# Optimization experiments

Measured on AMD Instinct MI355X. Metric: run time of the kernel, lower is better.

The kernel has to match this reference:

```python
import jax, jax.numpy as jnp
import numpy as np

B, S, E = 2, 2048, 1024
H, KV = 16, 4
D = E // H            # head_dim = 64
N_REP = H // KV       # 4
WIN = 256             # window_size
KV_DIM = KV * D       # 256


def setup_inputs() -> dict:
    key = jax.random.key(0)
    ks = jax.random.split(key, 10)
    sc_e = 1.0 / np.sqrt(E)
    return {
        "x":  jax.random.normal(ks[0], (B, S, E), jnp.float32),
        # weights stored as [in, out] (transposed torch Linear weight)
        "wq": jax.random.normal(ks[1], (E, E), jnp.float32) * sc_e,
        "bq": jax.random.normal(ks[2], (E,), jnp.float32) * 0.01,
        "wk": jax.random.normal(ks[3], (E, KV_DIM), jnp.float32) * sc_e,
        "bk": jax.random.normal(ks[4], (KV_DIM,), jnp.float32) * 0.01,
        "wv": jax.random.normal(ks[5], (E, KV_DIM), jnp.float32) * sc_e,
        "bv": jax.random.normal(ks[6], (KV_DIM,), jnp.float32) * 0.01,
        "wo": jax.random.normal(ks[7], (E, E), jnp.float32) * sc_e,
        "bo": jax.random.normal(ks[8], (E,), jnp.float32) * 0.01,
    }


def reference(x, wq, bq, wk, bk, wv, bv, wo, bo):
    b, s, _ = x.shape
    q = (x @ wq + bq).reshape(b, s, H, D).transpose(0, 2, 1, 3)    # [B,H,S,D]
    k = (x @ wk + bk).reshape(b, s, KV, D).transpose(0, 2, 1, 3)   # [B,KV,S,D]
    v = (x @ wv + bv).reshape(b, s, KV, D).transpose(0, 2, 1, 3)
    # repeat_kv: each kv head repeated N_REP times consecutively
    k = jnp.repeat(k, N_REP, axis=1)                               # [B,H,S,D]
    v = jnp.repeat(v, N_REP, axis=1)
    scores = jnp.einsum("bhqd,bhkd->bhqk", q, k) * (D ** -0.5)    # [B,H,S,S]
    i = jnp.arange(s)[:, None]
    j = jnp.arange(s)[None, :]
    masked = (j > i) | ((i - j) > WIN)  # True = masked (causal sliding window)
    scores = jnp.where(masked[None, None], -jnp.inf, scores)
    attn = jax.nn.softmax(scores, axis=-1)
    ctx = jnp.einsum("bhqk,bhkd->bhqd", attn, v)                   # [B,H,S,D]
    ctx = ctx.transpose(0, 2, 1, 3).reshape(b, s, E)
    return ctx @ wo + bo
```

## Files before the change

### kernel.cpp

```cpp
#include <hip/hip_runtime.h>
#include <stdint.h>

typedef unsigned short u16;
typedef __attribute__((ext_vector_type(8))) __bf16 bf16x8;
typedef __attribute__((ext_vector_type(4))) __bf16 bf16x4;
typedef __attribute__((ext_vector_type(4))) float f32x4;

#define S_LEN 2048
#define EMB   1024
#define NH    16
#define NKV   4
#define HD    64
#define WIN   256
#define NB    2
#define MROWS (NB * S_LEN)
#define PPAD  72

__device__ __forceinline__ u16 f2bf(float f) {
    uint32_t u = __float_as_uint(f);
    uint32_t r = (u + 0x7FFFu + ((u >> 16) & 1u)) >> 16;
    return (u16)r;
}

__device__ __forceinline__ float fast_exp2(float x) {
#if __has_builtin(__builtin_amdgcn_exp2f)
    return __builtin_amdgcn_exp2f(x);
#else
    float r; asm("v_exp_f32 %0, %1" : "=v"(r) : "v"(x)); return r;
#endif
}

__device__ __forceinline__ void gload16(const void* g, void* l) {
    __builtin_amdgcn_global_load_lds(
        (const __attribute__((address_space(1))) uint32_t*)(uintptr_t)g,
        (__attribute__((address_space(3))) uint32_t*)(uintptr_t)l,
        16, 0, 0);
}

__device__ __forceinline__ void transpose_job64(const float* __restrict__ in,
                                                u16* __restrict__ out,
                                                int R, int C, int bx, int by, int tid) {
    __shared__ float t[64][33];
    int c0 = bx * 32, r0 = by * 64;
    int tx = tid & 31, ty = tid >> 5;
#pragma unroll
    for (int j = 0; j < 64; j += 8)
        t[ty + j][tx] = in[(size_t)(r0 + ty + j) * C + (c0 + tx)];
    __syncthreads();
#pragma unroll
    for (int j = 0; j < 32; j += 8) {
        int c = j + ty;
        uint32_t v = f2bf(t[2 * tx][c]) | ((uint32_t)f2bf(t[2 * tx + 1][c]) << 16);
        *(uint32_t*)(out + (size_t)(c0 + c) * R + r0 + 2 * tx) = v;
    }
}

__global__ __launch_bounds__(256) void prep_kernel(
    const float* __restrict__ x,  const float* __restrict__ wq,
    const float* __restrict__ wk, const float* __restrict__ wv,
    const float* __restrict__ wo,
    u16* __restrict__ xb, u16* __restrict__ wqt, u16* __restrict__ wkt,
    u16* __restrict__ wvt, u16* __restrict__ wot) {
    int bid = blockIdx.x, tid = threadIdx.x;
    if (bid < 2048) {
        int i = bid * 256 + tid;
        const float4* p = (const float4*)x + (size_t)i * 2;
        float4 a = p[0], b = p[1];
        uint4 q;
        q.x = f2bf(a.x) | ((uint32_t)f2bf(a.y) << 16);
        q.y = f2bf(a.z) | ((uint32_t)f2bf(a.w) << 16);
        q.z = f2bf(b.x) | ((uint32_t)f2bf(b.y) << 16);
        q.w = f2bf(b.z) | ((uint32_t)f2bf(b.w) << 16);
        ((uint4*)xb)[i] = q;
    } else if (bid < 2560) {
        int lb = bid - 2048;  transpose_job64(wq, wqt, EMB, EMB, lb & 31, lb >> 5, tid);
    } else if (bid < 2688) {
        int lb = bid - 2560;  transpose_job64(wk, wkt, EMB, 256, lb & 7, lb >> 3, tid);
    } else if (bid < 2816) {
        int lb = bid - 2688;  transpose_job64(wv, wvt, EMB, 256, lb & 7, lb >> 3, tid);
    } else {
        int lb = bid - 2816;  transpose_job64(wo, wot, EMB, EMB, lb & 31, lb >> 5, tid);
    }
}

__device__ __forceinline__ void gemm_core64(const __bf16* __restrict__ A, const __bf16* __restrict__ Bt,
                                            int K, int m0, int n0r,
                                            __bf16 (*As)[64 * 64], __bf16 (*Bs)[128 * 64],
                                            f32x4 (&acc)[2][4], int tid) {
    const int lane = tid & 63, w = tid >> 6;
    const int wr = w >> 1, wc = w & 1;
    const int r = lane & 15, g = lane >> 4;

    auto stage = [&](int buf, int k0) {
#pragma unroll
        for (int i = 0; i < 2; ++i) {
            int chunk = (w * 2 + i) * 64 + lane;
            int row = chunk >> 3, cc = chunk & 7;
            gload16(A + (size_t)(m0 + row) * K + k0 + cc * 8, &As[buf][(w * 2 + i) * 512]);
        }
#pragma unroll
        for (int i = 0; i < 4; ++i) {
            int chunk = (w * 4 + i) * 64 + lane;
            int row = chunk >> 3, cc = chunk & 7;
            gload16(Bt + (size_t)(n0r + row) * K + k0 + cc * 8, &Bs[buf][(w * 4 + i) * 512]);
        }
    };

    stage(0, 0);
    __syncthreads();
    for (int k0 = 0; k0 < K; k0 += 64) {
        int cur = (k0 >> 6) & 1;
        if (k0 + 64 < K) stage(cur ^ 1, k0 + 64);
        bf16x8 af[2][2], bfr[4][2];
#pragma unroll
        for (int mf = 0; mf < 2; ++mf)
#pragma unroll
            for (int kk = 0; kk < 2; ++kk)
                af[mf][kk] = *(const bf16x8*)(&As[cur][(wr * 32 + mf * 16 + r) * 64 + kk * 32 + g * 8]);
#pragma unroll
        for (int nf = 0; nf < 4; ++nf)
#pragma unroll
            for (int kk = 0; kk < 2; ++kk)
                bfr[nf][kk] = *(const bf16x8*)(&Bs[cur][(wc * 64 + nf * 16 + r) * 64 + kk * 32 + g * 8]);
#pragma unroll
        for (int mf = 0; mf < 2; ++mf)
#pragma unroll
            for (int nf = 0; nf < 4; ++nf)
#pragma unroll
                for (int kk = 0; kk < 2; ++kk)
                    acc[mf][nf] = __builtin_amdgcn_mfma_f32_16x16x32_bf16(
                        af[mf][kk], bfr[nf][kk], acc[mf][nf], 0, 0, 0);
        __syncthreads();
    }
}

__global__ __launch_bounds__(256, 3) void gemm_qkv_kernel(
    const __bf16* __restrict__ xb, const __bf16* __restrict__ wqt,
    const __bf16* __restrict__ wkt, const __bf16* __restrict__ wvt,
    const float* __restrict__ bq, const float* __restrict__ bk, const float* __restrict__ bv,
    __bf16* __restrict__ Qb, __bf16* __restrict__ Kb, __bf16* __restrict__ Vblk) {
    __shared__ __align__(16) __bf16 As[2][64 * 64];
    __shared__ __align__(16) __bf16 Bs[2][128 * 64];
    int tid = threadIdx.x;
    int wg = (blockIdx.x & 7) * 96 + (blockIdx.x >> 3);
    int n0 = (wg % 12) * 128, m0 = (wg / 12) * 64;

    const __bf16* Bt; int n0r; const float* bias; int mode;
    if (n0 < 1024)      { Bt = wqt; n0r = n0;        bias = bq; mode = 0; }
    else if (n0 < 1280) { Bt = wkt; n0r = n0 - 1024; bias = bk; mode = 1; }
    else                { Bt = wvt; n0r = n0 - 1280; bias = bv; mode = 2; }

    f32x4 acc[2][4];
    f32x4 z = {0.f, 0.f, 0.f, 0.f};
#pragma unroll
    for (int i = 0; i < 2; ++i)
#pragma unroll
        for (int j = 0; j < 4; ++j) acc[i][j] = z;

    gemm_core64(xb, Bt, EMB, m0, n0r, As, Bs, acc, tid);

    const int lane = tid & 63, w = tid >> 6;
    const int wr = w >> 1, wc = w & 1, r = lane & 15, g = lane >> 4;
#pragma unroll
    for (int nf = 0; nf < 4; ++nf) {
        int nn = n0r + wc * 64 + nf * 16 + r;
        float bb = bias[nn];
        int hh = nn >> 6, dd = nn & 63;
        if (mode == 2) {
#pragma unroll
            for (int mf = 0; mf < 2; ++mf) {
                int s0 = m0 + wr * 32 + mf * 16 + g * 4;
                int bi = s0 >> 11, s = s0 & 2047;
                bf16x4 pk;
#pragma unroll
                for (int reg = 0; reg < 4; ++reg) pk[reg] = (__bf16)(acc[mf][nf][reg] + bb);
                *reinterpret_cast<bf16x4*>(Vblk + (size_t)(bi * NKV + hh) * (S_LEN * HD)
                                           + (s >> 6) * 4096 + dd * 64 + (s & 63)) = pk;
            }
        } else {
#pragma unroll
            for (int mf = 0; mf < 2; ++mf)
#pragma unroll
                for (int reg = 0; reg < 4; ++reg) {
                    int m = m0 + wr * 32 + mf * 16 + g * 4 + reg;
                    int bi = m >> 11, s = m & 2047;
                    __bf16 o = (__bf16)(acc[mf][nf][reg] + bb);
                    if (mode == 0)
                        Qb[((size_t)(bi * NH + hh) * S_LEN + s) * HD + dd] = o;
                    else
                        Kb[((size_t)(bi * NKV + hh) * S_LEN + s) * HD + dd] = o;
                }
        }
    }
}

__global__ __launch_bounds__(256, 3) void attn_kernel(const __bf16* __restrict__ Qb,
                                                      const __bf16* __restrict__ Kb,
                                                      const __bf16* __restrict__ Vblk,
                                                      __bf16* __restrict__ ctx) {
    __shared__ __align__(16) __bf16 Ks[2][64 * 64];
    __shared__ __align__(16) __bf16 Vs[2][64 * 64];
    __shared__ __align__(16) __bf16 Plds[4][16 * PPAD];
    const int tid = threadIdx.x;
    const int lane = tid & 63, w = tid >> 6;
    const int r = lane & 15, g = lane >> 4;
    const int q0 = blockIdx.x * 64;
    const int h = blockIdx.y, b = blockIdx.z;
    const int kvh = h >> 2;
    const __bf16* Qw = Qb + ((size_t)(b * NH + h) * S_LEN + q0 + w * 16) * HD;
    const __bf16* Kh = Kb + (size_t)(b * NKV + kvh) * S_LEN * HD;
    const __bf16* Vh = Vblk + (size_t)(b * NKV + kvh) * S_LEN * HD;
    __bf16* Pw = &Plds[w][0];

    const int n0s = w * 128 + lane;
    const int n1s = n0s + 64;
    const int srcoff0 = (n0s >> 3) * 64 + (((n0s & 7) ^ ((n0s >> 3) & 7)) * 8);
    const int srcoff1 = (n1s >> 3) * 64 + (((n1s & 7) ^ ((n1s >> 3) & 7)) * 8);
    const int dst0 = (w * 2) * 512;
    const int dst1 = dst0 + 512;

    auto stage = [&](int buf, int kbase) {
        const __bf16* Kt = Kh + (size_t)kbase * 64;
        const __bf16* Vt = Vh + (size_t)kbase * 64;
        gload16(Kt + srcoff0, &Ks[buf][dst0]);
        gload16(Kt + srcoff1, &Ks[buf][dst1]);
        gload16(Vt + srcoff0, &Vs[buf][dst0]);
        gload16(Vt + srcoff1, &Vs[buf][dst1]);
    };

    const int swz0 = ((0 * 4 + g) ^ (r & 7)) * 8;
    const int swz1 = ((1 * 4 + g) ^ (r & 7)) * 8;

    bf16x8 qf[2];
#pragma unroll
    for (int kk = 0; kk < 2; ++kk)
        qf[kk] = *(const bf16x8*)(Qw + r * 64 + kk * 32 + g * 8);

    f32x4 z = {0.f, 0.f, 0.f, 0.f};
    f32x4 o[4];
#pragma unroll
    for (int i = 0; i < 4; ++i) o[i] = z;
    float psum = 0.f;

    const float SC = 0.18033688011112042f;
    const int iq = q0 + w * 16 + r;

    auto tile = [&](int buf, int kbase, bool masked) {
        const __bf16* Kl = &Ks[buf][0];
        const __bf16* Vl = &Vs[buf][0];
        bf16x8 kf[4][2];
#pragma unroll
        for (int nf = 0; nf < 4; ++nf) {
            kf[nf][0] = *(const bf16x8*)(Kl + nf * 1024 + r * 64 + swz0);
            kf[nf][1] = *(const bf16x8*)(Kl + nf * 1024 + r * 64 + swz1);
        }
        f32x4 sa[4];
#pragma unroll
        for (int nf = 0; nf < 4; ++nf) sa[nf] = z;
#pragma unroll
        for (int nf = 0; nf < 4; ++nf)
#pragma unroll
            for (int kk = 0; kk < 2; ++kk)
                sa[nf] = __builtin_amdgcn_mfma_f32_16x16x32_bf16(kf[nf][kk], qf[kk], sa[nf], 0, 0, 0);
#pragma unroll
        for (int nf = 0; nf < 4; ++nf) {
            int jb = kbase + nf * 16 + g * 4;
            bf16x4 pk;
#pragma unroll
            for (int reg = 0; reg < 4; ++reg) {
                float x = sa[nf][reg] * SC;
                if (masked) {
                    uint32_t d = (uint32_t)(iq - (jb + reg));
                    x = (d <= (uint32_t)WIN) ? x : -1e30f;
                }
                float e = fast_exp2(x);
                psum += e;
                pk[reg] = (__bf16)e;
            }
            *reinterpret_cast<bf16x4*>(Pw + r * PPAD + nf * 16 + g * 4) = pk;
        }
        bf16x8 vf[4][2];
#pragma unroll
        for (int nf2 = 0; nf2 < 4; ++nf2) {
            vf[nf2][0] = *(const bf16x8*)(Vl + nf2 * 1024 + r * 64 + swz0);
            vf[nf2][1] = *(const bf16x8*)(Vl + nf2 * 1024 + r * 64 + swz1);
        }
#pragma unroll
        for (int kk2 = 0; kk2 < 2; ++kk2) {
            bf16x8 pa = *(const bf16x8*)(Pw + r * PPAD + kk2 * 32 + g * 8);
#pragma unroll
            for (int nf2 = 0; nf2 < 4; ++nf2)
                o[nf2] = __builtin_amdgcn_mfma_f32_16x16x32_bf16(vf[nf2][kk2], pa, o[nf2], 0, 0, 0);
        }
    };

    const int kb0 = (q0 >= 256) ? (q0 - 256) : 0;
    const int nt = (q0 - kb0) / 64 + 1;
    stage(0, kb0);
    __syncthreads();
    for (int t = 0; t < nt; ++t) {
        int kbase = kb0 + t * 64;
        if (t + 1 < nt) stage((t + 1) & 1, kbase + 64);
        bool masked = (kbase == q0) || (q0 >= 256 && t == 0);
        tile(t & 1, kbase, masked);
        __syncthreads();
    }

    psum += __shfl_xor(psum, 16, 64);
    psum += __shfl_xor(psum, 32, 64);
    float linv = 1.0f / psum;

    int s = q0 + w * 16 + r;
#pragma unroll
    for (int nf2 = 0; nf2 < 4; ++nf2) {
        bf16x4 pk;
#pragma unroll
        for (int reg = 0; reg < 4; ++reg) pk[reg] = (__bf16)(o[nf2][reg] * linv);
        *reinterpret_cast<bf16x4*>(ctx + ((size_t)(b * S_LEN + s)) * EMB + h * 64 + nf2 * 16 + g * 4) = pk;
    }
}

__global__ __launch_bounds__(256, 3) void gemm_out_kernel(const __bf16* __restrict__ ctxb,
                                                          const __bf16* __restrict__ wot,
                                                          const float* __restrict__ bo,
                                                          float* __restrict__ out) {
    __shared__ __align__(16) __bf16 As[2][64 * 64];
    __shared__ __align__(16) __bf16 Bs[2][128 * 64];
    int tid = threadIdx.x;
    int wg = (blockIdx.x & 7) * 64 + (blockIdx.x >> 3);
    int n0 = (wg % 8) * 128, m0 = (wg / 8) * 64;

    f32x4 acc[2][4];
    f32x4 z = {0.f, 0.f, 0.f, 0.f};
#pragma unroll
    for (int i = 0; i < 2; ++i)
#pragma unroll
        for (int j = 0; j < 4; ++j) acc[i][j] = z;

    gemm_core64(ctxb, wot, EMB, m0, n0, As, Bs, acc, tid);

    const int lane = tid & 63, w = tid >> 6;
    const int wr = w >> 1, wc = w & 1, r = lane & 15, g = lane >> 4;
#pragma unroll
    for (int nf = 0; nf < 4; ++nf) {
        int n = n0 + wc * 64 + nf * 16 + r;
        float bb = bo[n];
#pragma unroll
        for (int mf = 0; mf < 2; ++mf)
#pragma unroll
            for (int reg = 0; reg < 4; ++reg) {
                int m = m0 + wr * 32 + mf * 16 + g * 4 + reg;
                out[(size_t)m * EMB + n] = acc[mf][nf][reg] + bb;
            }
    }
}

extern "C" void kernel_launch(void* const* d_in, const int* in_sizes, int n_in,
                              void* d_out, int out_size, void* d_ws, size_t ws_size,
                              hipStream_t stream) {
    const float* x  = (const float*)d_in[0];
    const float* wq = (const float*)d_in[1];
    const float* bq = (const float*)d_in[2];
    const float* wk = (const float*)d_in[3];
    const float* bk = (const float*)d_in[4];
    const float* wv = (const float*)d_in[5];
    const float* bv = (const float*)d_in[6];
    const float* wo = (const float*)d_in[7];
    const float* bo = (const float*)d_in[8];
    float* out = (float*)d_out;

    char* ws = (char*)d_ws;
    __bf16* xb   = (__bf16*)ws;          ws += (size_t)MROWS * EMB * 2;
    __bf16* wqt  = (__bf16*)ws;          ws += (size_t)EMB * EMB * 2;
    __bf16* wkt  = (__bf16*)ws;          ws += (size_t)256 * EMB * 2;
    __bf16* wvt  = (__bf16*)ws;          ws += (size_t)256 * EMB * 2;
    __bf16* wot  = (__bf16*)ws;          ws += (size_t)EMB * EMB * 2;
    __bf16* Qb   = (__bf16*)ws;          ws += (size_t)NB * NH * S_LEN * HD * 2;
    __bf16* Kb   = (__bf16*)ws;          ws += (size_t)NB * NKV * S_LEN * HD * 2;
    __bf16* Vblk = (__bf16*)ws;          ws += (size_t)NB * NKV * S_LEN * HD * 2;
    __bf16* ctx  = (__bf16*)ws;          ws += (size_t)MROWS * EMB * 2;

    prep_kernel<<<3328, 256, 0, stream>>>(x, wq, wk, wv, wo,
                                          (u16*)xb, (u16*)wqt, (u16*)wkt, (u16*)wvt, (u16*)wot);
    gemm_qkv_kernel<<<768, 256, 0, stream>>>(xb, wqt, wkt, wvt, bq, bk, bv, Qb, Kb, Vblk);
    attn_kernel<<<dim3(32, 16, 2), 256, 0, stream>>>(Qb, Kb, Vblk, ctx);
    gemm_out_kernel<<<512, 256, 0, stream>>>(ctx, wot, bo, out);
}
```

Baseline: 66.51 us.

## Fuse x bf16 conversion into QKV GEMM and double query rows per attention block

The separate fp32-to-bf16 pass over x in the prep kernel is removed. The QKV GEMM now loads fp32 x into registers, converts it and writes bf16 into shared memory inside its pipelined loop, saving a full write and re-read of xb. Separately, the attention kernel now processes 128 queries per block (two 16-row groups per wave), so each staged K/V tile is reused across twice as many queries. The cost is more registers, more K tiles per block, masking applied on every tile, and half as many attention blocks.

```diff
diff --git a/kernel.cpp b/kernel.cpp
--- a/kernel.cpp
+++ b/kernel.cpp
@@ -56,30 +56,19 @@
 }
 
 __global__ __launch_bounds__(256) void prep_kernel(
-    const float* __restrict__ x,  const float* __restrict__ wq,
-    const float* __restrict__ wk, const float* __restrict__ wv,
-    const float* __restrict__ wo,
-    u16* __restrict__ xb, u16* __restrict__ wqt, u16* __restrict__ wkt,
+    const float* __restrict__ wq, const float* __restrict__ wk,
+    const float* __restrict__ wv, const float* __restrict__ wo,
+    u16* __restrict__ wqt, u16* __restrict__ wkt,
     u16* __restrict__ wvt, u16* __restrict__ wot) {
     int bid = blockIdx.x, tid = threadIdx.x;
-    if (bid < 2048) {
-        int i = bid * 256 + tid;
-        const float4* p = (const float4*)x + (size_t)i * 2;
-        float4 a = p[0], b = p[1];
-        uint4 q;
-        q.x = f2bf(a.x) | ((uint32_t)f2bf(a.y) << 16);
-        q.y = f2bf(a.z) | ((uint32_t)f2bf(a.w) << 16);
-        q.z = f2bf(b.x) | ((uint32_t)f2bf(b.y) << 16);
-        q.w = f2bf(b.z) | ((uint32_t)f2bf(b.w) << 16);
-        ((uint4*)xb)[i] = q;
-    } else if (bid < 2560) {
-        int lb = bid - 2048;  transpose_job64(wq, wqt, EMB, EMB, lb & 31, lb >> 5, tid);
-    } else if (bid < 2688) {
-        int lb = bid - 2560;  transpose_job64(wk, wkt, EMB, 256, lb & 7, lb >> 3, tid);
-    } else if (bid < 2816) {
-        int lb = bid - 2688;  transpose_job64(wv, wvt, EMB, 256, lb & 7, lb >> 3, tid);
+    if (bid < 512) {
+        int lb = bid;         transpose_job64(wq, wqt, EMB, EMB, lb & 31, lb >> 5, tid);
+    } else if (bid < 640) {
+        int lb = bid - 512;   transpose_job64(wk, wkt, EMB, 256, lb & 7, lb >> 3, tid);
+    } else if (bid < 768) {
+        int lb = bid - 640;   transpose_job64(wv, wvt, EMB, 256, lb & 7, lb >> 3, tid);
     } else {
-        int lb = bid - 2816;  transpose_job64(wo, wot, EMB, EMB, lb & 31, lb >> 5, tid);
+        int lb = bid - 768;   transpose_job64(wo, wot, EMB, EMB, lb & 31, lb >> 5, tid);
     }
 }
 
@@ -135,7 +124,7 @@
 }
 
 __global__ __launch_bounds__(256, 3) void gemm_qkv_kernel(
-    const __bf16* __restrict__ xb, const __bf16* __restrict__ wqt,
+    const float* __restrict__ x, const __bf16* __restrict__ wqt,
     const __bf16* __restrict__ wkt, const __bf16* __restrict__ wvt,
     const float* __restrict__ bq, const float* __restrict__ bk, const float* __restrict__ bv,
     __bf16* __restrict__ Qb, __bf16* __restrict__ Kb, __bf16* __restrict__ Vblk) {
@@ -150,6 +139,35 @@
     else if (n0 < 1280) { Bt = wkt; n0r = n0 - 1024; bias = bk; mode = 1; }
     else                { Bt = wvt; n0r = n0 - 1280; bias = bv; mode = 2; }
 
+    const int lane = tid & 63, w = tid >> 6;
+    const int wr = w >> 1, wc = w & 1, r = lane & 15, g = lane >> 4;
+
+    const int arow = tid >> 2, aq4 = tid & 3;
+    const float* Ax = x + (size_t)(m0 + arow) * EMB + aq4 * 16;
+    const int aoff = arow * 64 + aq4 * 16;
+
+    auto issueA = [&](float4 (&ar)[4], int k0) {
+        const float4* p = (const float4*)(Ax + k0);
+        ar[0] = p[0]; ar[1] = p[1]; ar[2] = p[2]; ar[3] = p[3];
+    };
+    auto writeA = [&](float4 (&ar)[4], int buf) {
+        bf16x8 h0, h1;
+        h0[0] = (__bf16)ar[0].x; h0[1] = (__bf16)ar[0].y; h0[2] = (__bf16)ar[0].z; h0[3] = (__bf16)ar[0].w;
+        h0[4] = (__bf16)ar[1].x; h0[5] = (__bf16)ar[1].y; h0[6] = (__bf16)ar[1].z; h0[7] = (__bf16)ar[1].w;
+        h1[0] = (__bf16)ar[2].x; h1[1] = (__bf16)ar[2].y; h1[2] = (__bf16)ar[2].z; h1[3] = (__bf16)ar[2].w;
+        h1[4] = (__bf16)ar[3].x; h1[5] = (__bf16)ar[3].y; h1[6] = (__bf16)ar[3].z; h1[7] = (__bf16)ar[3].w;
+        *(bf16x8*)(&As[buf][aoff]) = h0;
+        *(bf16x8*)(&As[buf][aoff + 8]) = h1;
+    };
+    auto stageB = [&](int buf, int k0) {
+#pragma unroll
+        for (int i = 0; i < 4; ++i) {
+            int chunk = (w * 4 + i) * 64 + lane;
+            int row = chunk >> 3, cc = chunk & 7;
+            gload16(Bt + (size_t)(n0r + row) * EMB + k0 + cc * 8, &Bs[buf][(w * 4 + i) * 512]);
+        }
+    };
+
     f32x4 acc[2][4];
     f32x4 z = {0.f, 0.f, 0.f, 0.f};
 #pragma unroll
@@ -157,10 +175,39 @@
 #pragma unroll
         for (int j = 0; j < 4; ++j) acc[i][j] = z;
 
-    gemm_core64(xb, Bt, EMB, m0, n0r, As, Bs, acc, tid);
-
-    const int lane = tid & 63, w = tid >> 6;
-    const int wr = w >> 1, wc = w & 1, r = lane & 15, g = lane >> 4;
+    float4 ar[4];
+    issueA(ar, 0);
+    stageB(0, 0);
+    writeA(ar, 0);
+    __syncthreads();
+    for (int k0 = 0; k0 < EMB; k0 += 64) {
+        int cur = (k0 >> 6) & 1;
+        bool more = (k0 + 64) < EMB;
+        if (more) { issueA(ar, k0 + 64); stageB(cur ^ 1, k0 + 64); }
+        __builtin_amdgcn_sched_barrier(0);
+        bf16x8 af[2][2], bfr[4][2];
+#pragma unroll
+        for (int mf = 0; mf < 2; ++mf)
+#pragma unroll
+            for (int kk = 0; kk < 2; ++kk)
+                af[mf][kk] = *(const bf16x8*)(&As[cur][(wr * 32 + mf * 16 + r) * 64 + kk * 32 + g * 8]);
+#pragma unroll
+        for (int nf = 0; nf < 4; ++nf)
+#pragma unroll
+            for (int kk = 0; kk < 2; ++kk)
+                bfr[nf][kk] = *(const bf16x8*)(&Bs[cur][(wc * 64 + nf * 16 + r) * 64 + kk * 32 + g * 8]);
+#pragma unroll
+        for (int mf = 0; mf < 2; ++mf)
+#pragma unroll
+            for (int nf = 0; nf < 4; ++nf)
+#pragma unroll
+                for (int kk = 0; kk < 2; ++kk)
+                    acc[mf][nf] = __builtin_amdgcn_mfma_f32_16x16x32_bf16(
+                        af[mf][kk], bfr[nf][kk], acc[mf][nf], 0, 0, 0);
+        if (more) writeA(ar, cur ^ 1);
+        __syncthreads();
+    }
+
 #pragma unroll
     for (int nf = 0; nf < 4; ++nf) {
         int nn = n0r + wc * 64 + nf * 16 + r;
@@ -200,14 +247,13 @@
                                                       __bf16* __restrict__ ctx) {
     __shared__ __align__(16) __bf16 Ks[2][64 * 64];
     __shared__ __align__(16) __bf16 Vs[2][64 * 64];
-    __shared__ __align__(16) __bf16 Plds[4][16 * PPAD];
+    __shared__ __align__(16) __bf16 Plds[4][32 * PPAD];
     const int tid = threadIdx.x;
     const int lane = tid & 63, w = tid >> 6;
     const int r = lane & 15, g = lane >> 4;
-    const int q0 = blockIdx.x * 64;
+    const int q0 = blockIdx.x * 128;
     const int h = blockIdx.y, b = blockIdx.z;
     const int kvh = h >> 2;
-    const __bf16* Qw = Qb + ((size_t)(b * NH + h) * S_LEN + q0 + w * 16) * HD;
     const __bf16* Kh = Kb + (size_t)(b * NKV + kvh) * S_LEN * HD;
     const __bf16* Vh = Vblk + (size_t)(b * NKV + kvh) * S_LEN * HD;
     __bf16* Pw = &Plds[w][0];
@@ -231,92 +277,100 @@
     const int swz0 = ((0 * 4 + g) ^ (r & 7)) * 8;
     const int swz1 = ((1 * 4 + g) ^ (r & 7)) * 8;
 
-    bf16x8 qf[2];
-#pragma unroll
-    for (int kk = 0; kk < 2; ++kk)
-        qf[kk] = *(const bf16x8*)(Qw + r * 64 + kk * 32 + g * 8);
+    bf16x8 qf[2][2];
+#pragma unroll
+    for (int gq = 0; gq < 2; ++gq)
+#pragma unroll
+        for (int kk = 0; kk < 2; ++kk)
+            qf[gq][kk] = *(const bf16x8*)(Qb + ((size_t)(b * NH + h) * S_LEN
+                                          + q0 + w * 32 + gq * 16 + r) * HD + kk * 32 + g * 8);
 
     f32x4 z = {0.f, 0.f, 0.f, 0.f};
-    f32x4 o[4];
-#pragma unroll
-    for (int i = 0; i < 4; ++i) o[i] = z;
-    float psum = 0.f;
+    f32x4 o[2][4];
+#pragma unroll
+    for (int gq = 0; gq < 2; ++gq)
+#pragma unroll
+        for (int i = 0; i < 4; ++i) o[gq][i] = z;
+    float psum[2] = {0.f, 0.f};
 
     const float SC = 0.18033688011112042f;
-    const int iq = q0 + w * 16 + r;
-
-    auto tile = [&](int buf, int kbase, bool masked) {
+    int iq[2];
+#pragma unroll
+    for (int gq = 0; gq < 2; ++gq) iq[gq] = q0 + w * 32 + gq * 16 + r;
+
+    auto tile = [&](int buf, int kbase) {
         const __bf16* Kl = &Ks[buf][0];
         const __bf16* Vl = &Vs[buf][0];
-        bf16x8 kf[4][2];
+        f32x4 sa[2][4];
+#pragma unroll
+        for (int gq = 0; gq < 2; ++gq)
+#pragma unroll
+            for (int nf = 0; nf < 4; ++nf) sa[gq][nf] = z;
 #pragma unroll
         for (int nf = 0; nf < 4; ++nf) {
-            kf[nf][0] = *(const bf16x8*)(Kl + nf * 1024 + r * 64 + swz0);
-            kf[nf][1] = *(const bf16x8*)(Kl + nf * 1024 + r * 64 + swz1);
-        }
-        f32x4 sa[4];
-#pragma unroll
-        for (int nf = 0; nf < 4; ++nf) sa[nf] = z;
-#pragma unroll
-        for (int nf = 0; nf < 4; ++nf)
-#pragma unroll
-            for (int kk = 0; kk < 2; ++kk)
-                sa[nf] = __builtin_amdgcn_mfma_f32_16x16x32_bf16(kf[nf][kk], qf[kk], sa[nf], 0, 0, 0);
-#pragma unroll
-        for (int nf = 0; nf < 4; ++nf) {
-            int jb = kbase + nf * 16 + g * 4;
-            bf16x4 pk;
-#pragma unroll
-            for (int reg = 0; reg < 4; ++reg) {
-                float x = sa[nf][reg] * SC;
-                if (masked) {
-                    uint32_t d = (uint32_t)(iq - (jb + reg));
+            bf16x8 kf0 = *(const bf16x8*)(Kl + nf * 1024 + r * 64 + swz0);
+            bf16x8 kf1 = *(const bf16x8*)(Kl + nf * 1024 + r * 64 + swz1);
+            sa[0][nf] = __builtin_amdgcn_mfma_f32_16x16x32_bf16(kf0, qf[0][0], sa[0][nf], 0, 0, 0);
+            sa[1][nf] = __builtin_amdgcn_mfma_f32_16x16x32_bf16(kf0, qf[1][0], sa[1][nf], 0, 0, 0);
+            sa[0][nf] = __builtin_amdgcn_mfma_f32_16x16x32_bf16(kf1, qf[0][1], sa[0][nf], 0, 0, 0);
+            sa[1][nf] = __builtin_amdgcn_mfma_f32_16x16x32_bf16(kf1, qf[1][1], sa[1][nf], 0, 0, 0);
+        }
+#pragma unroll
+        for (int gq = 0; gq < 2; ++gq)
+#pragma unroll
+            for (int nf = 0; nf < 4; ++nf) {
+                int jb = kbase + nf * 16 + g * 4;
+                bf16x4 pk;
+#pragma unroll
+                for (int reg = 0; reg < 4; ++reg) {
+                    float x = sa[gq][nf][reg] * SC;
+                    uint32_t d = (uint32_t)(iq[gq] - (jb + reg));
                     x = (d <= (uint32_t)WIN) ? x : -1e30f;
+                    float e = fast_exp2(x);
+                    psum[gq] += e;
+                    pk[reg] = (__bf16)e;
                 }
-                float e = fast_exp2(x);
-                psum += e;
-                pk[reg] = (__bf16)e;
+                *reinterpret_cast<bf16x4*>(Pw + gq * 16 * PPAD + r * PPAD + nf * 16 + g * 4) = pk;
             }
-            *reinterpret_cast<bf16x4*>(Pw + r * PPAD + nf * 16 + g * 4) = pk;
-        }
-        bf16x8 vf[4][2];
-#pragma unroll
-        for (int nf2 = 0; nf2 < 4; ++nf2) {
-            vf[nf2][0] = *(const bf16x8*)(Vl + nf2 * 1024 + r * 64 + swz0);
-            vf[nf2][1] = *(const bf16x8*)(Vl + nf2 * 1024 + r * 64 + swz1);
-        }
 #pragma unroll
         for (int kk2 = 0; kk2 < 2; ++kk2) {
-            bf16x8 pa = *(const bf16x8*)(Pw + r * PPAD + kk2 * 32 + g * 8);
-#pragma unroll
-            for (int nf2 = 0; nf2 < 4; ++nf2)
-                o[nf2] = __builtin_amdgcn_mfma_f32_16x16x32_bf16(vf[nf2][kk2], pa, o[nf2], 0, 0, 0);
+            bf16x8 pa0 = *(const bf16x8*)(Pw + r * PPAD + kk2 * 32 + g * 8);
+            bf16x8 pa1 = *(const bf16x8*)(Pw + 16 * PPAD + r * PPAD + kk2 * 32 + g * 8);
+            int sw = kk2 ? swz1 : swz0;
+#pragma unroll
+            for (int nf2 = 0; nf2 < 4; ++nf2) {
+                bf16x8 vf = *(const bf16x8*)(Vl + nf2 * 1024 + r * 64 + sw);
+                o[0][nf2] = __builtin_amdgcn_mfma_f32_16x16x32_bf16(vf, pa0, o[0][nf2], 0, 0, 0);
+                o[1][nf2] = __builtin_amdgcn_mfma_f32_16x16x32_bf16(vf, pa1, o[1][nf2], 0, 0, 0);
+            }
         }
     };
 
     const int kb0 = (q0 >= 256) ? (q0 - 256) : 0;
-    const int nt = (q0 - kb0) / 64 + 1;
+    const int nt = (q0 + 64 - kb0) / 64 + 1;
     stage(0, kb0);
     __syncthreads();
     for (int t = 0; t < nt; ++t) {
         int kbase = kb0 + t * 64;
         if (t + 1 < nt) stage((t + 1) & 1, kbase + 64);
-        bool masked = (kbase == q0) || (q0 >= 256 && t == 0);
-        tile(t & 1, kbase, masked);
+        tile(t & 1, kbase);
         __syncthreads();
     }
 
-    psum += __shfl_xor(psum, 16, 64);
-    psum += __shfl_xor(psum, 32, 64);
-    float linv = 1.0f / psum;
-
-    int s = q0 + w * 16 + r;
-#pragma unroll
-    for (int nf2 = 0; nf2 < 4; ++nf2) {
-        bf16x4 pk;
-#pragma unroll
-        for (int reg = 0; reg < 4; ++reg) pk[reg] = (__bf16)(o[nf2][reg] * linv);
-        *reinterpret_cast<bf16x4*>(ctx + ((size_t)(b * S_LEN + s)) * EMB + h * 64 + nf2 * 16 + g * 4) = pk;
+#pragma unroll
+    for (int gq = 0; gq < 2; ++gq) {
+        psum[gq] += __shfl_xor(psum[gq], 16, 64);
+        psum[gq] += __shfl_xor(psum[gq], 32, 64);
+        float linv = 1.0f / psum[gq];
+        int s = q0 + w * 32 + gq * 16 + r;
+#pragma unroll
+        for (int nf2 = 0; nf2 < 4; ++nf2) {
+            bf16x4 pk;
+#pragma unroll
+            for (int reg = 0; reg < 4; ++reg) pk[reg] = (__bf16)(o[gq][nf2][reg] * linv);
+            *reinterpret_cast<bf16x4*>(ctx + ((size_t)(b * S_LEN + s)) * EMB
+                                       + h * 64 + nf2 * 16 + g * 4) = pk;
+        }
     }
 }
 
@@ -370,7 +424,6 @@
     float* out = (float*)d_out;
 
     char* ws = (char*)d_ws;
-    __bf16* xb   = (__bf16*)ws;          ws += (size_t)MROWS * EMB * 2;
     __bf16* wqt  = (__bf16*)ws;          ws += (size_t)EMB * EMB * 2;
     __bf16* wkt  = (__bf16*)ws;          ws += (size_t)256 * EMB * 2;
     __bf16* wvt  = (__bf16*)ws;          ws += (size_t)256 * EMB * 2;
@@ -380,9 +433,9 @@
     __bf16* Vblk = (__bf16*)ws;          ws += (size_t)NB * NKV * S_LEN * HD * 2;
     __bf16* ctx  = (__bf16*)ws;          ws += (size_t)MROWS * EMB * 2;
 
-    prep_kernel<<<3328, 256, 0, stream>>>(x, wq, wk, wv, wo,
-                                          (u16*)xb, (u16*)wqt, (u16*)wkt, (u16*)wvt, (u16*)wot);
-    gemm_qkv_kernel<<<768, 256, 0, stream>>>(xb, wqt, wkt, wvt, bq, bk, bv, Qb, Kb, Vblk);
-    attn_kernel<<<dim3(32, 16, 2), 256, 0, stream>>>(Qb, Kb, Vblk, ctx);
+    prep_kernel<<<1280, 256, 0, stream>>>(wq, wk, wv, wo,
+                                          (u16*)wqt, (u16*)wkt, (u16*)wvt, (u16*)wot);
+    gemm_qkv_kernel<<<768, 256, 0, stream>>>(x, wqt, wkt, wvt, bq, bk, bv, Qb, Kb, Vblk);
+    attn_kernel<<<dim3(16, 16, 2), 256, 0, stream>>>(Qb, Kb, Vblk, ctx);
     gemm_out_kernel<<<512, 256, 0, stream>>>(ctx, wot, bo, out);
 }
```

Measured after the change: 74.00 us. +11.3%, slower.

## Process 128 query rows per attention block to reuse K/V tiles

Applied to the files above, without the earlier changes.

Each attention workgroup now handles 128 queries (32 per wavefront, two 16-row groups) instead of 64, so every K and V fragment read from LDS feeds two MFMAs and each staged K/V tile serves twice as many queries. The grid is halved and the tile loop gains one extra 64-key tile. The window mask is now applied on every tile instead of only the edge tiles. This costs more registers and LDS for P, and the smaller grid (512 blocks) may reduce occupancy and load balance on the GPU.

```diff
diff --git a/kernel.cpp b/kernel.cpp
--- a/kernel.cpp
+++ b/kernel.cpp
@@ -200,14 +200,13 @@
                                                       __bf16* __restrict__ ctx) {
     __shared__ __align__(16) __bf16 Ks[2][64 * 64];
     __shared__ __align__(16) __bf16 Vs[2][64 * 64];
-    __shared__ __align__(16) __bf16 Plds[4][16 * PPAD];
+    __shared__ __align__(16) __bf16 Plds[4][32 * PPAD];
     const int tid = threadIdx.x;
     const int lane = tid & 63, w = tid >> 6;
     const int r = lane & 15, g = lane >> 4;
-    const int q0 = blockIdx.x * 64;
+    const int q0 = blockIdx.x * 128;
     const int h = blockIdx.y, b = blockIdx.z;
     const int kvh = h >> 2;
-    const __bf16* Qw = Qb + ((size_t)(b * NH + h) * S_LEN + q0 + w * 16) * HD;
     const __bf16* Kh = Kb + (size_t)(b * NKV + kvh) * S_LEN * HD;
     const __bf16* Vh = Vblk + (size_t)(b * NKV + kvh) * S_LEN * HD;
     __bf16* Pw = &Plds[w][0];
@@ -231,92 +230,100 @@
     const int swz0 = ((0 * 4 + g) ^ (r & 7)) * 8;
     const int swz1 = ((1 * 4 + g) ^ (r & 7)) * 8;
 
-    bf16x8 qf[2];
-#pragma unroll
-    for (int kk = 0; kk < 2; ++kk)
-        qf[kk] = *(const bf16x8*)(Qw + r * 64 + kk * 32 + g * 8);
+    bf16x8 qf[2][2];
+#pragma unroll
+    for (int gq = 0; gq < 2; ++gq)
+#pragma unroll
+        for (int kk = 0; kk < 2; ++kk)
+            qf[gq][kk] = *(const bf16x8*)(Qb + ((size_t)(b * NH + h) * S_LEN
+                                          + q0 + w * 32 + gq * 16 + r) * HD + kk * 32 + g * 8);
 
     f32x4 z = {0.f, 0.f, 0.f, 0.f};
-    f32x4 o[4];
-#pragma unroll
-    for (int i = 0; i < 4; ++i) o[i] = z;
-    float psum = 0.f;
+    f32x4 o[2][4];
+#pragma unroll
+    for (int gq = 0; gq < 2; ++gq)
+#pragma unroll
+        for (int i = 0; i < 4; ++i) o[gq][i] = z;
+    float psum[2] = {0.f, 0.f};
 
     const float SC = 0.18033688011112042f;
-    const int iq = q0 + w * 16 + r;
-
-    auto tile = [&](int buf, int kbase, bool masked) {
+    int iq[2];
+#pragma unroll
+    for (int gq = 0; gq < 2; ++gq) iq[gq] = q0 + w * 32 + gq * 16 + r;
+
+    auto tile = [&](int buf, int kbase) {
         const __bf16* Kl = &Ks[buf][0];
         const __bf16* Vl = &Vs[buf][0];
-        bf16x8 kf[4][2];
+        f32x4 sa[2][4];
+#pragma unroll
+        for (int gq = 0; gq < 2; ++gq)
+#pragma unroll
+            for (int nf = 0; nf < 4; ++nf) sa[gq][nf] = z;
 #pragma unroll
         for (int nf = 0; nf < 4; ++nf) {
-            kf[nf][0] = *(const bf16x8*)(Kl + nf * 1024 + r * 64 + swz0);
-            kf[nf][1] = *(const bf16x8*)(Kl + nf * 1024 + r * 64 + swz1);
-        }
-        f32x4 sa[4];
-#pragma unroll
-        for (int nf = 0; nf < 4; ++nf) sa[nf] = z;
-#pragma unroll
-        for (int nf = 0; nf < 4; ++nf)
-#pragma unroll
-            for (int kk = 0; kk < 2; ++kk)
-                sa[nf] = __builtin_amdgcn_mfma_f32_16x16x32_bf16(kf[nf][kk], qf[kk], sa[nf], 0, 0, 0);
-#pragma unroll
-        for (int nf = 0; nf < 4; ++nf) {
-            int jb = kbase + nf * 16 + g * 4;
-            bf16x4 pk;
-#pragma unroll
-            for (int reg = 0; reg < 4; ++reg) {
-                float x = sa[nf][reg] * SC;
-                if (masked) {
-                    uint32_t d = (uint32_t)(iq - (jb + reg));
+            bf16x8 kf0 = *(const bf16x8*)(Kl + nf * 1024 + r * 64 + swz0);
+            bf16x8 kf1 = *(const bf16x8*)(Kl + nf * 1024 + r * 64 + swz1);
+            sa[0][nf] = __builtin_amdgcn_mfma_f32_16x16x32_bf16(kf0, qf[0][0], sa[0][nf], 0, 0, 0);
+            sa[1][nf] = __builtin_amdgcn_mfma_f32_16x16x32_bf16(kf0, qf[1][0], sa[1][nf], 0, 0, 0);
+            sa[0][nf] = __builtin_amdgcn_mfma_f32_16x16x32_bf16(kf1, qf[0][1], sa[0][nf], 0, 0, 0);
+            sa[1][nf] = __builtin_amdgcn_mfma_f32_16x16x32_bf16(kf1, qf[1][1], sa[1][nf], 0, 0, 0);
+        }
+#pragma unroll
+        for (int gq = 0; gq < 2; ++gq)
+#pragma unroll
+            for (int nf = 0; nf < 4; ++nf) {
+                int jb = kbase + nf * 16 + g * 4;
+                bf16x4 pk;
+#pragma unroll
+                for (int reg = 0; reg < 4; ++reg) {
+                    float x = sa[gq][nf][reg] * SC;
+                    uint32_t d = (uint32_t)(iq[gq] - (jb + reg));
                     x = (d <= (uint32_t)WIN) ? x : -1e30f;
+                    float e = fast_exp2(x);
+                    psum[gq] += e;
+                    pk[reg] = (__bf16)e;
                 }
-                float e = fast_exp2(x);
-                psum += e;
-                pk[reg] = (__bf16)e;
+                *reinterpret_cast<bf16x4*>(Pw + gq * 16 * PPAD + r * PPAD + nf * 16 + g * 4) = pk;
             }
-            *reinterpret_cast<bf16x4*>(Pw + r * PPAD + nf * 16 + g * 4) = pk;
-        }
-        bf16x8 vf[4][2];
-#pragma unroll
-        for (int nf2 = 0; nf2 < 4; ++nf2) {
-            vf[nf2][0] = *(const bf16x8*)(Vl + nf2 * 1024 + r * 64 + swz0);
-            vf[nf2][1] = *(const bf16x8*)(Vl + nf2 * 1024 + r * 64 + swz1);
-        }
 #pragma unroll
         for (int kk2 = 0; kk2 < 2; ++kk2) {
-            bf16x8 pa = *(const bf16x8*)(Pw + r * PPAD + kk2 * 32 + g * 8);
-#pragma unroll
-            for (int nf2 = 0; nf2 < 4; ++nf2)
-                o[nf2] = __builtin_amdgcn_mfma_f32_16x16x32_bf16(vf[nf2][kk2], pa, o[nf2], 0, 0, 0);
+            bf16x8 pa0 = *(const bf16x8*)(Pw + r * PPAD + kk2 * 32 + g * 8);
+            bf16x8 pa1 = *(const bf16x8*)(Pw + 16 * PPAD + r * PPAD + kk2 * 32 + g * 8);
+            int sw = kk2 ? swz1 : swz0;
+#pragma unroll
+            for (int nf2 = 0; nf2 < 4; ++nf2) {
+                bf16x8 vf = *(const bf16x8*)(Vl + nf2 * 1024 + r * 64 + sw);
+                o[0][nf2] = __builtin_amdgcn_mfma_f32_16x16x32_bf16(vf, pa0, o[0][nf2], 0, 0, 0);
+                o[1][nf2] = __builtin_amdgcn_mfma_f32_16x16x32_bf16(vf, pa1, o[1][nf2], 0, 0, 0);
+            }
         }
     };
 
     const int kb0 = (q0 >= 256) ? (q0 - 256) : 0;
-    const int nt = (q0 - kb0) / 64 + 1;
+    const int nt = (q0 + 64 - kb0) / 64 + 1;
     stage(0, kb0);
     __syncthreads();
     for (int t = 0; t < nt; ++t) {
         int kbase = kb0 + t * 64;
         if (t + 1 < nt) stage((t + 1) & 1, kbase + 64);
-        bool masked = (kbase == q0) || (q0 >= 256 && t == 0);
-        tile(t & 1, kbase, masked);
+        tile(t & 1, kbase);
         __syncthreads();
     }
 
-    psum += __shfl_xor(psum, 16, 64);
-    psum += __shfl_xor(psum, 32, 64);
-    float linv = 1.0f / psum;
-
-    int s = q0 + w * 16 + r;
-#pragma unroll
-    for (int nf2 = 0; nf2 < 4; ++nf2) {
-        bf16x4 pk;
-#pragma unroll
-        for (int reg = 0; reg < 4; ++reg) pk[reg] = (__bf16)(o[nf2][reg] * linv);
-        *reinterpret_cast<bf16x4*>(ctx + ((size_t)(b * S_LEN + s)) * EMB + h * 64 + nf2 * 16 + g * 4) = pk;
+#pragma unroll
+    for (int gq = 0; gq < 2; ++gq) {
+        psum[gq] += __shfl_xor(psum[gq], 16, 64);
+        psum[gq] += __shfl_xor(psum[gq], 32, 64);
+        float linv = 1.0f / psum[gq];
+        int s = q0 + w * 32 + gq * 16 + r;
+#pragma unroll
+        for (int nf2 = 0; nf2 < 4; ++nf2) {
+            bf16x4 pk;
+#pragma unroll
+            for (int reg = 0; reg < 4; ++reg) pk[reg] = (__bf16)(o[gq][nf2][reg] * linv);
+            *reinterpret_cast<bf16x4*>(ctx + ((size_t)(b * S_LEN + s)) * EMB
+                                       + h * 64 + nf2 * 16 + g * 4) = pk;
+        }
     }
 }
 
@@ -383,6 +390,6 @@
     prep_kernel<<<3328, 256, 0, stream>>>(x, wq, wk, wv, wo,
                                           (u16*)xb, (u16*)wqt, (u16*)wkt, (u16*)wvt, (u16*)wot);
     gemm_qkv_kernel<<<768, 256, 0, stream>>>(xb, wqt, wkt, wvt, bq, bk, bv, Qb, Kb, Vblk);
-    attn_kernel<<<dim3(32, 16, 2), 256, 0, stream>>>(Qb, Kb, Vblk, ctx);
+    attn_kernel<<<dim3(16, 16, 2), 256, 0, stream>>>(Qb, Kb, Vblk, ctx);
     gemm_out_kernel<<<512, 256, 0, stream>>>(ctx, wot, bo, out);
 }
```

Measured after the change: 66.16 us, median of 2. Within noise of the previous version (-0.5%).
